# Optimization experiments

Hardware: AMD Instinct MI355X
Metric: run time of the kernel (lower is better)

The kernel has to match this reference:

```python
import jax, jax.numpy as jnp
import numpy as np

B, T, IN, H, L, OUT = 64, 512, 128, 256, 3, 50
G = 3 * H  # gate dim (r,z,n)


def setup_inputs() -> dict:
    key = jax.random.key(0)
    ks = jax.random.split(key, 18)
    s = 0.08  # keep gates out of saturation
    r = jax.random.normal
    return {
        "x": r(ks[0], (B, T, IN), jnp.float32),
        "Wih0": r(ks[1], (2, G, IN)) * s,
        "Whh0": r(ks[2], (2, G, H)) * s,
        "bih0": r(ks[3], (2, G)) * s,
        "bhh0": r(ks[4], (2, G)) * s,
        "Wih": r(ks[5], (L - 1, 2, G, 2 * H)) * s,
        "Whh": r(ks[6], (L - 1, 2, G, H)) * s,
        "bih": r(ks[7], (L - 1, 2, G)) * s,
        "bhh": r(ks[8], (L - 1, 2, G)) * s,
        "W1": r(ks[9], (128, 2 * H)) * s,
        "b1": r(ks[10], (128,)) * s,
        "W2": r(ks[11], (64, 128)) * s,
        "b2": r(ks[12], (64,)) * s,
        "W3": r(ks[13], (H, 64)) * s,
        "b3": r(ks[14], (H,)) * s,
        "W4": r(ks[15], (OUT, H)) * s,
        "b4": r(ks[16], (OUT,)) * s,
    }


def _gru_dir(x, Wih, Whh, bih, bhh, reverse):
    # x: [B,T,D]. Precompute input gates with one big GEMM, scan only hidden matmul.
    xg = jnp.einsum('btd,gd->tbg', x, Wih) + bih  # [T,B,3H]
    h0 = jnp.zeros((x.shape[0], H), x.dtype)

    def step(h, xg_t):
        hg = h @ Whh.T + bhh                     # [B,3H]
        xr, xz, xn = jnp.split(xg_t, 3, axis=-1)
        hr, hz, hn = jnp.split(hg, 3, axis=-1)
        r = jax.nn.sigmoid(xr + hr)
        z = jax.nn.sigmoid(xz + hz)
        n = jnp.tanh(xn + r * hn)
        h = (1.0 - z) * n + z * h
        return h, h

    _, ys = jax.lax.scan(step, h0, xg, reverse=reverse)  # ys[t] aligned to time t
    return jnp.transpose(ys, (1, 0, 2))  # [B,T,H]


def reference(x, Wih0, Whh0, bih0, bhh0, Wih, Whh, bih, bhh,
              W1, b1, W2, b2, W3, b3, W4, b4):
    h = x
    for l in range(L):
        if l == 0:
            wi, wh, bi, bh = Wih0, Whh0, bih0, bhh0
        else:
            wi, wh, bi, bh = Wih[l - 1], Whh[l - 1], bih[l - 1], bhh[l - 1]
        fwd = _gru_dir(h, wi[0], wh[0], bi[0], bh[0], False)
        bwd = _gru_dir(h, wi[1], wh[1], bi[1], bh[1], True)
        h = jnp.concatenate([fwd, bwd], axis=-1)  # [B,T,2H]
    last = h[:, -1, :]  # [B,2H]
    y = jax.nn.relu(last @ W1.T + b1)
    y = jax.nn.relu(y @ W2.T + b2)
    y = jax.nn.relu(y @ W3.T + b3)
    return y @ W4.T + b4  # [B,OUT]
```

## Files before the change

### kernel.cpp

```cpp
#include <hip/hip_runtime.h>
#include <stdint.h>

#define B_ 64
#define T_ 512
#define IN_ 128
#define H_ 256
#define G_ 768
#define M0_ (B_*T_)

typedef _Float16 f16;
typedef _Float16 f16x2 __attribute__((ext_vector_type(2)));
typedef _Float16 half8 __attribute__((ext_vector_type(8)));
typedef float f32x4 __attribute__((ext_vector_type(4)));

#if __has_builtin(__builtin_amdgcn_fdot2)
__device__ inline float fdot2f(f16x2 a, f16x2 b, float c){ return __builtin_amdgcn_fdot2(a, b, c, false); }
#else
__device__ inline float fdot2f(f16x2 a, f16x2 b, float c){ return c + (float)a.x*(float)b.x + (float)a.y*(float)b.y; }
#endif

template<bool AF32>
__global__ __launch_bounds__(256) void k_proj(
    const float* __restrict__ Af, const f16* __restrict__ Ah,
    const float* __restrict__ W, const float* __restrict__ bias,
    f16* __restrict__ out, int K)
{
  int dir = blockIdx.z;
  const float* Wd = W + (size_t)dir*G_*K;
  const float* bd = bias + dir*G_;
  f16* outd = out + (size_t)dir*M0_*G_;
  int m0 = blockIdx.x*128, n0 = blockIdx.y*128;
  int tid = threadIdx.x, lane = tid & 63, wv = tid >> 6;
  int wm = wv >> 1, wn = wv & 1;
  int l15 = lane & 15, quad = lane >> 4;

  __shared__ f16 As[128][72];
  __shared__ f16 Ws[128][72];

  f32x4 acc[4][4];
  #pragma unroll
  for (int i = 0; i < 4; i++)
    #pragma unroll
    for (int j = 0; j < 4; j++) acc[i][j] = (f32x4){0.f,0.f,0.f,0.f};

  int lr = tid >> 3, lk = (tid & 7) * 8;
  for (int k0 = 0; k0 < K; k0 += 64){
    #pragma unroll
    for (int it = 0; it < 4; it++){
      int row = lr + it*32;
      if (AF32){
        const float* p = &Af[(size_t)(m0+row)*K + k0 + lk];
        float4 v0 = *(const float4*)p;
        float4 v1 = *(const float4*)(p + 4);
        *(half8*)&As[row][lk] = (half8){(f16)v0.x,(f16)v0.y,(f16)v0.z,(f16)v0.w,
                                        (f16)v1.x,(f16)v1.y,(f16)v1.z,(f16)v1.w};
      } else {
        *(uint4*)&As[row][lk] = *(const uint4*)&Ah[(size_t)(m0+row)*K + k0 + lk];
      }
      {
        const float* p = &Wd[(size_t)(n0+row)*K + k0 + lk];
        float4 v0 = *(const float4*)p;
        float4 v1 = *(const float4*)(p + 4);
        *(half8*)&Ws[row][lk] = (half8){(f16)v0.x,(f16)v0.y,(f16)v0.z,(f16)v0.w,
                                        (f16)v1.x,(f16)v1.y,(f16)v1.z,(f16)v1.w};
      }
    }
    __syncthreads();
    #pragma unroll
    for (int kk = 0; kk < 64; kk += 32){
      half8 af[4], bf[4];
      #pragma unroll
      for (int mi = 0; mi < 4; mi++) af[mi] = *(const half8*)&As[wm*64 + mi*16 + l15][kk + quad*8];
      #pragma unroll
      for (int ni = 0; ni < 4; ni++) bf[ni] = *(const half8*)&Ws[wn*64 + ni*16 + l15][kk + quad*8];
      #pragma unroll
      for (int mi = 0; mi < 4; mi++)
        #pragma unroll
        for (int ni = 0; ni < 4; ni++)
          acc[mi][ni] = __builtin_amdgcn_mfma_f32_16x16x32_f16(af[mi], bf[ni], acc[mi][ni], 0, 0, 0);
    }
    __syncthreads();
  }
  #pragma unroll
  for (int mi = 0; mi < 4; mi++){
    #pragma unroll
    for (int ni = 0; ni < 4; ni++){
      int m = m0 + wm*64 + mi*16 + quad*4;
      int n = n0 + wn*64 + ni*16 + l15;
      float bn = bd[n];
      #pragma unroll
      for (int r = 0; r < 4; r++)
        outd[(size_t)(m+r)*G_ + n] = (f16)(acc[mi][ni][r] + bn);
    }
  }
}

__global__ __launch_bounds__(512) __attribute__((amdgpu_waves_per_eu(2, 2)))
void k_rnn(
    const f16* __restrict__ xg, const float* __restrict__ whh,
    const float* __restrict__ bhh, f16* __restrict__ y)
{
  int b = blockIdx.x, dir = blockIdx.y;
  int tid = threadIdx.x, lane = tid & 63, wv = tid >> 6;
  int g = lane >> 4;
  int i = lane & 15;
  int u = wv*32 + (lane & 31);
  int dsel = (lane >> 4) & 1;

  const f16* cxg = xg + ((size_t)dir*M0_ + (size_t)b*T_)*G_;
  const float* wbase = whh + (size_t)dir*G_*H_;
  const float* bh = bhh + dir*G_;
  f16* yb = y + (size_t)b*T_*512 + dir*256;

  __shared__ __align__(16) f16 h0buf[256];
  __shared__ __align__(16) f16 h1buf[256];

  f16x2 wf2[192];
  #pragma unroll
  for (int m = 0; m < 6; m++){
    int gamma = m >> 1, d = m & 1;
    const float* wrow = wbase + (size_t)(gamma*256 + wv*32 + i + d*16)*H_ + g*64;
    #pragma unroll
    for (int q = 0; q < 16; q++){
      float4 v = ((const float4*)wrow)[q];
      wf2[m*32 + q*2 + 0] = (f16x2){(f16)v.x, (f16)v.y};
      wf2[m*32 + q*2 + 1] = (f16x2){(f16)v.z, (f16)v.w};
    }
  }

  float br = bh[u], bz = bh[u+256], bn = bh[u+512];
  float hreg = 0.f;
  if (tid < 256) h0buf[tid] = (f16)0.f;
  __syncthreads();

  f16 axr, axz, axn;
  {
    int t0 = dir ? (T_-1) : 0;
    const f16* xp = cxg + (size_t)t0*G_ + u;
    axr = xp[0]; axz = xp[256]; axn = xp[512];
  }

#define RSTEP(SRC, DST, TT, TN)                                                 \
  {                                                                             \
    const half8* hp = (const half8*)&SRC[g*64];                                 \
    float ac0=0.f, ac1=0.f, ac2=0.f, ac3=0.f, ac4=0.f, ac5=0.f;                 \
    half8 hcur = hp[0];                                                         \
    half8 hnxt = hp[1];                                                         \
    _Pragma("unroll")                                                           \
    for (int s2 = 0; s2 < 8; s2++){                                             \
      half8 hh = hcur;                                                          \
      hcur = hnxt;                                                              \
      if (s2 < 6) hnxt = hp[s2+2];                                              \
      _Pragma("unroll")                                                         \
      for (int q = 0; q < 4; q++){                                              \
        f16x2 pp = {hh[2*q], hh[2*q+1]};                                        \
        ac0 = fdot2f(wf2[0*32 + s2*4 + q], pp, ac0);                            \
        ac1 = fdot2f(wf2[1*32 + s2*4 + q], pp, ac1);                            \
        ac2 = fdot2f(wf2[2*32 + s2*4 + q], pp, ac2);                            \
        ac3 = fdot2f(wf2[3*32 + s2*4 + q], pp, ac3);                            \
        ac4 = fdot2f(wf2[4*32 + s2*4 + q], pp, ac4);                            \
        ac5 = fdot2f(wf2[5*32 + s2*4 + q], pp, ac5);                            \
      }                                                                         \
    }                                                                           \
    ac0 += __shfl_xor(ac0, 16); ac0 += __shfl_xor(ac0, 32);                     \
    ac1 += __shfl_xor(ac1, 16); ac1 += __shfl_xor(ac1, 32);                     \
    ac2 += __shfl_xor(ac2, 16); ac2 += __shfl_xor(ac2, 32);                     \
    ac3 += __shfl_xor(ac3, 16); ac3 += __shfl_xor(ac3, 32);                     \
    ac4 += __shfl_xor(ac4, 16); ac4 += __shfl_xor(ac4, 32);                     \
    ac5 += __shfl_xor(ac5, 16); ac5 += __shfl_xor(ac5, 32);                     \
    float sr = dsel ? ac1 : ac0;                                                \
    float sz = dsel ? ac3 : ac2;                                                \
    float sn = dsel ? ac5 : ac4;                                                \
    float ar = (float)axr + sr + br; ar = fminf(fmaxf(ar, -30.f), 30.f);        \
    float az = (float)axz + sz + bz; az = fminf(fmaxf(az, -30.f), 30.f);        \
    float r_ = 1.f/(1.f + __expf(-ar));                                         \
    float z_ = 1.f/(1.f + __expf(-az));                                         \
    float an = (float)axn + r_*(sn + bn); an = fminf(fmaxf(an, -15.f), 15.f);   \
    float e_ = __expf(2.f*an);                                                  \
    float nn = (e_ - 1.f)/(e_ + 1.f);                                           \
    hreg = (1.f - z_)*nn + z_*hreg;                                             \
    if (lane < 32){                                                             \
      DST[u] = (f16)hreg;                                                       \
      yb[(size_t)(TT)*512 + u] = (f16)hreg;                                     \
    }                                                                           \
    {           \
      const f16* xq = cxg + (size_t)(TN)*G_ + u;                                \
      axr = xq[0]; axz = xq[256]; axn = xq[512];                                \
    }                                                                           \
    asm volatile("s_waitcnt lgkmcnt(0)\n\ts_barrier" ::: "memory");             \
  }

  for (int s = 0; s < T_; s += 2){
    int ttA = dir ? (T_-1-s) : s;
    int ttB = dir ? (T_-2-s) : (s+1);
    int s2c = (s + 2 < T_) ? (s + 2) : (T_ - 1);
    int ttC = dir ? (T_-1-s2c) : s2c;

    RSTEP(h0buf, h1buf, ttA, ttB)
    RSTEP(h1buf, h0buf, ttB, ttC)
  }
#undef RSTEP
}

__global__ __launch_bounds__(256) void k_head(
    const f16* __restrict__ y,
    const float* __restrict__ W1, const float* __restrict__ b1,
    const float* __restrict__ W2, const float* __restrict__ b2,
    const float* __restrict__ W3, const float* __restrict__ b3,
    const float* __restrict__ W4, const float* __restrict__ b4,
    float* __restrict__ out)
{
  int b = blockIdx.x, tid = threadIdx.x;
  __shared__ float a0[512], a1[128], a2[64], a3[256];
  const f16* yr = y + ((size_t)b*T_ + (T_-1))*512;
  a0[tid] = (float)yr[tid]; a0[tid+256] = (float)yr[tid+256];
  __syncthreads();
  if (tid < 128){
    float s = b1[tid];
    const float4* w = (const float4*)(W1 + (size_t)tid*512);
    #pragma unroll 8
    for (int c = 0; c < 128; c++){
      float4 v = w[c];
      s += v.x*a0[c*4] + v.y*a0[c*4+1] + v.z*a0[c*4+2] + v.w*a0[c*4+3];
    }
    a1[tid] = fmaxf(s, 0.f);
  }
  __syncthreads();
  if (tid < 64){
    float s = b2[tid];
    const float4* w = (const float4*)(W2 + (size_t)tid*128);
    #pragma unroll
    for (int c = 0; c < 32; c++){
      float4 v = w[c];
      s += v.x*a1[c*4] + v.y*a1[c*4+1] + v.z*a1[c*4+2] + v.w*a1[c*4+3];
    }
    a2[tid] = fmaxf(s, 0.f);
  }
  __syncthreads();
  if (tid < 256){
    float s = b3[tid];
    const float4* w = (const float4*)(W3 + (size_t)tid*64);
    #pragma unroll
    for (int c = 0; c < 16; c++){
      float4 v = w[c];
      s += v.x*a2[c*4] + v.y*a2[c*4+1] + v.z*a2[c*4+2] + v.w*a2[c*4+3];
    }
    a3[tid] = fmaxf(s, 0.f);
  }
  __syncthreads();
  if (tid < 50){
    float s = b4[tid];
    const float4* w = (const float4*)(W4 + (size_t)tid*256);
    #pragma unroll
    for (int c = 0; c < 64; c++){
      float4 v = w[c];
      s += v.x*a3[c*4] + v.y*a3[c*4+1] + v.z*a3[c*4+2] + v.w*a3[c*4+3];
    }
    out[b*50 + tid] = s;
  }
}

extern "C" void kernel_launch(void* const* d_in, const int* in_sizes, int n_in,
                              void* d_out, int out_size, void* d_ws, size_t ws_size,
                              hipStream_t stream)
{
  const float* x    = (const float*)d_in[0];
  const float* Wih0 = (const float*)d_in[1];
  const float* Whh0 = (const float*)d_in[2];
  const float* bih0 = (const float*)d_in[3];
  const float* bhh0 = (const float*)d_in[4];
  const float* Wih  = (const float*)d_in[5];
  const float* Whh  = (const float*)d_in[6];
  const float* bih  = (const float*)d_in[7];
  const float* bhh  = (const float*)d_in[8];
  const float* W1 = (const float*)d_in[9];
  const float* b1 = (const float*)d_in[10];
  const float* W2 = (const float*)d_in[11];
  const float* b2 = (const float*)d_in[12];
  const float* W3 = (const float*)d_in[13];
  const float* b3 = (const float*)d_in[14];
  const float* W4 = (const float*)d_in[15];
  const float* b4 = (const float*)d_in[16];

  char* ws = (char*)d_ws;
  f16* xg = (f16*)ws;
  f16* y  = (f16*)(ws + 100663296ull);

  k_proj<true ><<<dim3(M0_/128, 6, 2), dim3(256), 0, stream>>>(x, nullptr, Wih0, bih0, xg, IN_);
  k_rnn        <<<dim3(B_, 2),         dim3(512), 0, stream>>>(xg, Whh0, bhh0, y);
  k_proj<false><<<dim3(M0_/128, 6, 2), dim3(256), 0, stream>>>(nullptr, y, Wih, bih, xg, 2*H_);
  k_rnn        <<<dim3(B_, 2),         dim3(512), 0, stream>>>(xg, Whh, bhh, y);
  k_proj<false><<<dim3(M0_/128, 6, 2), dim3(256), 0, stream>>>(nullptr, y, Wih + 1ull*2*G_*(2*H_), bih + 2*G_, xg, 2*H_);
  k_rnn        <<<dim3(B_, 2),         dim3(512), 0, stream>>>(xg, Whh + 1ull*2*G_*H_, bhh + 2*G_, y);

  k_head<<<dim3(B_), dim3(256), 0, stream>>>(y, W1, b1, W2, b2, W3, b3, W4, b4,
                                             (float*)d_out);
}
```

Before: 2.404 ms.

## Split recurrent matvec across 16 waves and skip unused last-layer output writes

The GRU recurrence kernel now runs with 1024 threads per block: each wave handles 16 hidden units instead of 32, so each lane holds 96 f16x2 weight registers instead of 192 and computes three dot products instead of six, with no dsel select. Twice as many waves share each step, which spreads the per-step dot-product latency at the cost of more barrier participants. A template flag also makes the last layer write its output only at timestep T-1, since the head reads only the final timestep. The backward direction of the last layer still writes its T-1 value, which is its first step, so the head's inputs are preserved.

Result: slower. 2.741 ms (+14.0%).

```diff
diff --git a/kernel.cpp b/kernel.cpp
--- a/kernel.cpp
+++ b/kernel.cpp
@@ -95,17 +95,16 @@
   }
 }
 
-__global__ __launch_bounds__(512) __attribute__((amdgpu_waves_per_eu(2, 2)))
+template<bool LASTL>
+__global__ __launch_bounds__(1024) __attribute__((amdgpu_waves_per_eu(4, 4)))
 void k_rnn(
     const f16* __restrict__ xg, const float* __restrict__ whh,
     const float* __restrict__ bhh, f16* __restrict__ y)
 {
   int b = blockIdx.x, dir = blockIdx.y;
   int tid = threadIdx.x, lane = tid & 63, wv = tid >> 6;
-  int g = lane >> 4;
-  int i = lane & 15;
-  int u = wv*32 + (lane & 31);
-  int dsel = (lane >> 4) & 1;
+  int i = lane & 15, q = lane >> 4;
+  int u = wv*16 + i;
 
   const f16* cxg = xg + ((size_t)dir*M0_ + (size_t)b*T_)*G_;
   const float* wbase = whh + (size_t)dir*G_*H_;
@@ -115,16 +114,15 @@
   __shared__ __align__(16) f16 h0buf[256];
   __shared__ __align__(16) f16 h1buf[256];
 
-  f16x2 wf2[192];
+  f16x2 wf[96];
   #pragma unroll
-  for (int m = 0; m < 6; m++){
-    int gamma = m >> 1, d = m & 1;
-    const float* wrow = wbase + (size_t)(gamma*256 + wv*32 + i + d*16)*H_ + g*64;
-    #pragma unroll
-    for (int q = 0; q < 16; q++){
-      float4 v = ((const float4*)wrow)[q];
-      wf2[m*32 + q*2 + 0] = (f16x2){(f16)v.x, (f16)v.y};
-      wf2[m*32 + q*2 + 1] = (f16x2){(f16)v.z, (f16)v.w};
+  for (int g = 0; g < 3; g++){
+    const float* wrow = wbase + (size_t)(g*256 + u)*H_ + q*64;
+    #pragma unroll
+    for (int j = 0; j < 16; j++){
+      float4 v = ((const float4*)wrow)[j];
+      wf[g*32 + j*2 + 0] = (f16x2){(f16)v.x, (f16)v.y};
+      wf[g*32 + j*2 + 1] = (f16x2){(f16)v.z, (f16)v.w};
     }
   }
 
@@ -142,8 +140,8 @@
 
 #define RSTEP(SRC, DST, TT, TN)                                                 \
   {                                                                             \
-    const half8* hp = (const half8*)&SRC[g*64];                                 \
-    float ac0=0.f, ac1=0.f, ac2=0.f, ac3=0.f, ac4=0.f, ac5=0.f;                 \
+    const half8* hp = (const half8*)&SRC[q*64];                                 \
+    float ac0 = 0.f, ac1 = 0.f, ac2 = 0.f;                                      \
     half8 hcur = hp[0];                                                         \
     half8 hnxt = hp[1];                                                         \
     _Pragma("unroll")                                                           \
@@ -152,38 +150,30 @@
       hcur = hnxt;                                                              \
       if (s2 < 6) hnxt = hp[s2+2];                                              \
       _Pragma("unroll")                                                         \
-      for (int q = 0; q < 4; q++){                                              \
-        f16x2 pp = {hh[2*q], hh[2*q+1]};                                        \
-        ac0 = fdot2f(wf2[0*32 + s2*4 + q], pp, ac0);                            \
-        ac1 = fdot2f(wf2[1*32 + s2*4 + q], pp, ac1);                            \
-        ac2 = fdot2f(wf2[2*32 + s2*4 + q], pp, ac2);                            \
-        ac3 = fdot2f(wf2[3*32 + s2*4 + q], pp, ac3);                            \
-        ac4 = fdot2f(wf2[4*32 + s2*4 + q], pp, ac4);                            \
-        ac5 = fdot2f(wf2[5*32 + s2*4 + q], pp, ac5);                            \
+      for (int e = 0; e < 4; e++){                                              \
+        f16x2 pp = {hh[2*e], hh[2*e+1]};                                        \
+        ac0 = fdot2f(wf[ 0 + s2*4 + e], pp, ac0);                               \
+        ac1 = fdot2f(wf[32 + s2*4 + e], pp, ac1);                               \
+        ac2 = fdot2f(wf[64 + s2*4 + e], pp, ac2);                               \
       }                                                                         \
     }                                                                           \
     ac0 += __shfl_xor(ac0, 16); ac0 += __shfl_xor(ac0, 32);                     \
     ac1 += __shfl_xor(ac1, 16); ac1 += __shfl_xor(ac1, 32);                     \
     ac2 += __shfl_xor(ac2, 16); ac2 += __shfl_xor(ac2, 32);                     \
-    ac3 += __shfl_xor(ac3, 16); ac3 += __shfl_xor(ac3, 32);                     \
-    ac4 += __shfl_xor(ac4, 16); ac4 += __shfl_xor(ac4, 32);                     \
-    ac5 += __shfl_xor(ac5, 16); ac5 += __shfl_xor(ac5, 32);                     \
-    float sr = dsel ? ac1 : ac0;                                                \
-    float sz = dsel ? ac3 : ac2;                                                \
-    float sn = dsel ? ac5 : ac4;                                                \
-    float ar = (float)axr + sr + br; ar = fminf(fmaxf(ar, -30.f), 30.f);        \
-    float az = (float)axz + sz + bz; az = fminf(fmaxf(az, -30.f), 30.f);        \
+    float ar = (float)axr + ac0 + br; ar = fminf(fmaxf(ar, -30.f), 30.f);       \
+    float az = (float)axz + ac1 + bz; az = fminf(fmaxf(az, -30.f), 30.f);       \
     float r_ = 1.f/(1.f + __expf(-ar));                                         \
     float z_ = 1.f/(1.f + __expf(-az));                                         \
-    float an = (float)axn + r_*(sn + bn); an = fminf(fmaxf(an, -15.f), 15.f);   \
+    float an = (float)axn + r_*(ac2 + bn); an = fminf(fmaxf(an, -15.f), 15.f);  \
     float e_ = __expf(2.f*an);                                                  \
     float nn = (e_ - 1.f)/(e_ + 1.f);                                           \
     hreg = (1.f - z_)*nn + z_*hreg;                                             \
-    if (lane < 32){                                                             \
+    if (lane < 16){                                                             \
       DST[u] = (f16)hreg;                                                       \
-      yb[(size_t)(TT)*512 + u] = (f16)hreg;                                     \
+      if (!LASTL || (TT) == T_-1)                                               \
+        yb[(size_t)(TT)*512 + u] = (f16)hreg;                                   \
     }                                                                           \
-    {           \
+    {          \
       const f16* xq = cxg + (size_t)(TN)*G_ + u;                                \
       axr = xq[0]; axz = xq[256]; axn = xq[512];                                \
     }                                                                           \
@@ -286,12 +276,12 @@
   f16* xg = (f16*)ws;
   f16* y  = (f16*)(ws + 100663296ull);
 
-  k_proj<true ><<<dim3(M0_/128, 6, 2), dim3(256), 0, stream>>>(x, nullptr, Wih0, bih0, xg, IN_);
-  k_rnn        <<<dim3(B_, 2),         dim3(512), 0, stream>>>(xg, Whh0, bhh0, y);
-  k_proj<false><<<dim3(M0_/128, 6, 2), dim3(256), 0, stream>>>(nullptr, y, Wih, bih, xg, 2*H_);
-  k_rnn        <<<dim3(B_, 2),         dim3(512), 0, stream>>>(xg, Whh, bhh, y);
-  k_proj<false><<<dim3(M0_/128, 6, 2), dim3(256), 0, stream>>>(nullptr, y, Wih + 1ull*2*G_*(2*H_), bih + 2*G_, xg, 2*H_);
-  k_rnn        <<<dim3(B_, 2),         dim3(512), 0, stream>>>(xg, Whh + 1ull*2*G_*H_, bhh + 2*G_, y);
+  k_proj<true >  <<<dim3(M0_/128, 6, 2), dim3(256),  0, stream>>>(x, nullptr, Wih0, bih0, xg, IN_);
+  k_rnn<false>   <<<dim3(B_, 2),         dim3(1024), 0, stream>>>(xg, Whh0, bhh0, y);
+  k_proj<false>  <<<dim3(M0_/128, 6, 2), dim3(256),  0, stream>>>(nullptr, y, Wih, bih, xg, 2*H_);
+  k_rnn<false>   <<<dim3(B_, 2),         dim3(1024), 0, stream>>>(xg, Whh, bhh, y);
+  k_proj<false>  <<<dim3(M0_/128, 6, 2), dim3(256),  0, stream>>>(nullptr, y, Wih + 1ull*2*G_*(2*H_), bih + 2*G_, xg, 2*H_);
+  k_rnn<true>    <<<dim3(B_, 2),         dim3(1024), 0, stream>>>(xg, Whh + 1ull*2*G_*H_, bhh + 2*G_, y);
 
   k_head<<<dim3(B_), dim3(256), 0, stream>>>(y, W1, b1, W2, b2, W3, b3, W4, b4,
                                              (float*)d_out);
```
